# Optimization experiments

Measured on AMD Instinct MI355X. Metric: run time of the kernel, lower is better.

The kernel has to match this reference:

```python
import jax, jax.numpy as jnp
import numpy as np

N = 20000   # nodes
E = 320000  # edges
D_IN = 256
D_OUT = 256


def setup_inputs() -> dict:
    key = jax.random.key(0)
    ks = jax.random.split(key, 12)
    s = 0.05
    return {
        "h": jax.random.normal(ks[0], (N, D_OUT), jnp.float32),
        "x": jax.random.normal(ks[1], (N, D_IN), jnp.float32),
        "pos": jax.random.normal(ks[2], (N, 3), jnp.float32),
        "W_fc": jax.random.normal(ks[3], (D_OUT, D_IN + D_OUT), jnp.float32) * s,
        "b_fc": jax.random.normal(ks[4], (D_OUT,), jnp.float32) * s,
        "W_conv": jax.random.normal(ks[5], (D_OUT, D_OUT), jnp.float32) * s,
        "W_ih": jax.random.normal(ks[6], (3 * D_OUT, D_OUT), jnp.float32) * s,
        "W_hh": jax.random.normal(ks[7], (3 * D_OUT, D_OUT), jnp.float32) * s,
        "b_ih": jax.random.normal(ks[8], (3 * D_OUT,), jnp.float32) * s,
        "b_hh": jax.random.normal(ks[9], (3 * D_OUT,), jnp.float32) * s,
        "edge_index_gate": jax.random.randint(ks[10], (2, E), 0, N, jnp.int64),
        "edge_index_cand": jax.random.randint(ks[11], (2, E), 0, N, jnp.int64),
    }


def reference(h, x, pos, W_fc, b_fc, W_conv, W_ih, W_hh, b_ih, b_hh,
              edge_index_gate, edge_index_cand):
    # fc + relu on concatenated [x, h]
    xh = jnp.concatenate([x, h], axis=-1)            # [N, in+out]
    xr = jax.nn.relu(xh @ W_fc.T + b_fc)             # [N, out]

    # GatedGraphConv, num_layers=1, aggr='add'
    m = xr @ W_conv                                  # [N, out]  (x @ weight[0])
    src, dst = edge_index_gate[0], edge_index_gate[1]
    agg = jax.ops.segment_sum(m[src], dst, num_segments=xr.shape[0])  # [N, out]

    # GRUCell(agg, xr)  (torch semantics: input=agg, hidden=xr)
    gi = agg @ W_ih.T + b_ih                         # [N, 3*out]
    gh = xr @ W_hh.T + b_hh                          # [N, 3*out]
    i_r, i_z, i_n = jnp.split(gi, 3, axis=-1)
    h_r, h_z, h_n = jnp.split(gh, 3, axis=-1)
    r = jax.nn.sigmoid(i_r + h_r)
    z = jax.nn.sigmoid(i_z + h_z)
    n = jnp.tanh(i_n + r * h_n)
    h_next = (1.0 - z) * n + z * xr
    return h_next
```

## Files before the change

kernel.cpp:

```cpp
#include <hip/hip_runtime.h>
#include <hip/hip_bf16.h>

#define N_NODES 20000
#define MPAD 20032
#define CAP 64

typedef __attribute__((ext_vector_type(8))) short short8;
typedef __attribute__((ext_vector_type(4))) float f32x4;

#define MFMA16(a,b,c) __builtin_amdgcn_mfma_f32_16x16x32_bf16(a,b,c,0,0,0)

#define FSW(r) (((r) & 3) ^ (((r) >> 2) & 3))

#define WAIT_BAR(NSTR) do { \
  asm volatile("s_waitcnt vmcnt(" NSTR ") lgkmcnt(0)" ::: "memory"); \
  __builtin_amdgcn_s_barrier(); \
  __builtin_amdgcn_sched_barrier(0); \
} while (0)
#define END_BAR() do { \
  __builtin_amdgcn_sched_barrier(0); \
  __builtin_amdgcn_s_barrier(); \
} while (0)

static __device__ __forceinline__ ushort f2bf(float f) {
  union { float f; uint u; } v; v.f = f;
  uint u = v.u;
  uint r = (u + 0x7FFFu + ((u >> 16) & 1u)) >> 16;
  return (ushort)r;
}
static __device__ __forceinline__ float bf2f(ushort s) {
  union { uint u; float f; } v; v.u = ((uint)s) << 16; return v.f;
}

typedef __attribute__((address_space(1))) const unsigned int guint;
typedef __attribute__((address_space(3))) unsigned int luint;
static __device__ __forceinline__ void gl2lds16(const void* g, void* l) {
  __builtin_amdgcn_global_load_lds((guint*)g, (luint*)l, 16, 0, 0);
}

static __device__ __forceinline__ void cvt8(const float* __restrict__ s, ushort* __restrict__ d) {
  float4 v0 = *(const float4*)s;
  float4 v1 = *(const float4*)(s + 4);
  union { ushort u[8]; uint4 v; } t;
  t.u[0]=f2bf(v0.x); t.u[1]=f2bf(v0.y); t.u[2]=f2bf(v0.z); t.u[3]=f2bf(v0.w);
  t.u[4]=f2bf(v1.x); t.u[5]=f2bf(v1.y); t.u[6]=f2bf(v1.z); t.u[7]=f2bf(v1.w);
  *(uint4*)d = t.v;
}

__global__ __launch_bounds__(256) void k_prep(
    const float* __restrict__ Wfc, const float* __restrict__ Wc,
    const float* __restrict__ Wih, const float* __restrict__ Whh,
    ushort* __restrict__ WfcB, ushort* __restrict__ WcB,
    ushort* __restrict__ WihB, ushort* __restrict__ Bg3, int* __restrict__ cnt) {
  int i = blockIdx.x * 256 + threadIdx.x;
  if (i < 16384) cvt8(Wfc + i * 8, WfcB + i * 8);
  if (i < 8192)  cvt8(Wc  + i * 8, WcB  + i * 8);
  if (i < 24576) cvt8(Wih + i * 8, WihB + i * 8);
  if (i < 24576) {
    int row = i >> 5;
    int k0 = (i & 31) * 8;
    int g = row / 48, rem = row - g * 48;
    int p = rem >> 4, ci = rem & 15;
    int c = g * 16 + ci;
    cvt8(Whh + ((size_t)(p * 256 + c)) * 256 + k0, Bg3 + (size_t)row * 512 + 256 + k0);
  }
  if (i < N_NODES) cnt[i] = 0;
}

__global__ __launch_bounds__(256, 4) void k_mid(
    const float* __restrict__ x, const float* __restrict__ h,
    const ushort* __restrict__ WfcB, const float* __restrict__ bfc,
    ushort* __restrict__ AX,
    const ushort* __restrict__ WihB, const ushort* __restrict__ WcB,
    ushort* __restrict__ Bg3,
    const int* __restrict__ eg, int* __restrict__ cnt, int* __restrict__ srcs) {
  __shared__ __attribute__((aligned(16))) ushort smem[4096];
  int bid = blockIdx.x;
  int t = threadIdx.x, w = t >> 6, l = t & 63;

  if (bid >= 1304) {
    int e = (bid - 1304) * 256 + t;
    if (e < 320000) {
      int d = eg[320000 + e];
      int slot = atomicAdd(&cnt[d], 1);
      if (slot < CAP) srcs[d * CAP + slot] = eg[e];
    }
    return;
  }

  if (bid >= 1256) {
    ushort* sA = smem;
    ushort* sB = smem + 2048;
    int wf = bid - 1256;
    int row0 = (wf % 12) * 64, col0 = (wf / 12) * 64;
    int wr = (w >> 1) * 32, wc = (w & 1) * 32;
    f32x4 acc[2][2] = {};
    for (int ks = 0; ks < 8; ++ks) {
      int k0 = ks * 32;
      {
        int r = t >> 2, wl = t & 3;
        int gw = wl ^ FSW(r);
        gl2lds16(WihB + (size_t)(row0 + r) * 256 + k0 + gw * 8,
                 (char*)sA + (size_t)(w * 64) * 16);
      }
      {
        int r = t >> 2, wl = t & 3;
        int gw = wl ^ FSW(r);
        gl2lds16(WcB + (size_t)(col0 + r) * 256 + k0 + gw * 8,
                 (char*)sB + (size_t)(w * 64) * 16);
      }
      __syncthreads();
      short8 af[2], bfr[2];
      #pragma unroll
      for (int mi = 0; mi < 2; ++mi) {
        int r = wr + mi * 16 + (l & 15);
        af[mi] = *(short8*)&sA[r * 32 + (((l >> 4)) ^ FSW(r)) * 8];
      }
      #pragma unroll
      for (int ni = 0; ni < 2; ++ni) {
        int br = wc + ni * 16 + (l & 15);
        bfr[ni] = *(short8*)&sB[br * 32 + (((l >> 4)) ^ FSW(br)) * 8];
      }
      #pragma unroll
      for (int mi = 0; mi < 2; ++mi)
        #pragma unroll
        for (int ni = 0; ni < 2; ++ni)
          acc[mi][ni] = MFMA16(af[mi], bfr[ni], acc[mi][ni]);
      __syncthreads();
    }
    #pragma unroll
    for (int mi = 0; mi < 2; ++mi)
      #pragma unroll
      for (int ni = 0; ni < 2; ++ni)
        #pragma unroll
        for (int q = 0; q < 4; ++q) {
          int jj = row0 + wr + mi*16 + (l>>4)*4 + q;
          int tc = col0 + wc + ni*16 + (l&15);
          int p = jj >> 8, c = jj & 255;
          int brow = (c >> 4) * 48 + p * 16 + (c & 15);
          Bg3[(size_t)brow * 512 + tc] = f2bf(acc[mi][ni][q]);
        }
    return;
  }

  ushort* sA = smem;
  ushort* sB = smem + 2048;
  int wk = (bid & 7) * 157 + (bid >> 3);
  int panel = wk >> 2, ch = wk & 3;
  if (panel >= 313) return;
  int row0 = panel * 64, col0 = ch * 64;
  int wr = (w >> 1) * 32, wc = (w & 1) * 32;
  int r_ = t >> 2, wl_ = t & 3;
  int gw_ = wl_ ^ FSW(r_);
  int gr_ = row0 + r_; if (gr_ > N_NODES - 1) gr_ = N_NODES - 1;

  f32x4 acc[2][2] = {};
  for (int ks = 0; ks < 16; ++ks) {
    int k0 = ks * 32;
    const float* Af = (ks < 8) ? x : h;
    int ka = k0 & 255;
    {
      union { ushort u[8]; uint4 v; } tmp;
      const float* p = Af + (size_t)gr_ * 256 + ka + gw_ * 8;
      float4 v0 = *(const float4*)p;
      float4 v1 = *(const float4*)(p + 4);
      tmp.u[0]=f2bf(v0.x); tmp.u[1]=f2bf(v0.y); tmp.u[2]=f2bf(v0.z); tmp.u[3]=f2bf(v0.w);
      tmp.u[4]=f2bf(v1.x); tmp.u[5]=f2bf(v1.y); tmp.u[6]=f2bf(v1.z); tmp.u[7]=f2bf(v1.w);
      *(uint4*)&sA[r_*32 + wl_*8] = tmp.v;
    }
    gl2lds16(WfcB + (size_t)(col0 + r_) * 512 + k0 + gw_ * 8,
             (char*)sB + (size_t)(w * 64) * 16);
    __syncthreads();
    short8 af[2], bfr[2];
    #pragma unroll
    for (int mi = 0; mi < 2; ++mi) {
      int r = wr + mi * 16 + (l & 15);
      af[mi] = *(short8*)&sA[r * 32 + (((l >> 4)) ^ FSW(r)) * 8];
    }
    #pragma unroll
    for (int ni = 0; ni < 2; ++ni) {
      int br = wc + ni * 16 + (l & 15);
      bfr[ni] = *(short8*)&sB[br * 32 + (((l >> 4)) ^ FSW(br)) * 8];
    }
    #pragma unroll
    for (int mi = 0; mi < 2; ++mi)
      #pragma unroll
      for (int ni = 0; ni < 2; ++ni)
        acc[mi][ni] = MFMA16(af[mi], bfr[ni], acc[mi][ni]);
    __syncthreads();
  }
  #pragma unroll
  for (int mi = 0; mi < 2; ++mi)
    #pragma unroll
    for (int ni = 0; ni < 2; ++ni)
      #pragma unroll
      for (int q = 0; q < 4; ++q) {
        int r = row0 + wr + mi*16 + (l>>4)*4 + q;
        int c = col0 + wc + ni*16 + (l&15);
        if (r < N_NODES) {
          float v = acc[mi][ni][q] + bfc[c];
          v = v > 0.f ? v : 0.f;
          AX[(size_t)r * 512 + 256 + c] = f2bf(v);
        }
      }
}

__global__ __launch_bounds__(256) void k_aggS(
    const int* __restrict__ cnt, const int* __restrict__ srcs,
    ushort* __restrict__ AX) {
  int node = blockIdx.x * 8 + (threadIdx.x >> 5);
  if (node >= N_NODES) return;
  int lane = threadIdx.x & 31;
  const int* bkt = srcs + node * CAP;
  int n = cnt[node]; if (n > CAP) n = CAP;
  float a[8] = {};
  int i = 0;
  for (; i + 4 <= n; i += 4) {
    uint4 v0 = *(const uint4*)(AX + (size_t)bkt[i  ] * 512 + 256 + lane * 8);
    uint4 v1 = *(const uint4*)(AX + (size_t)bkt[i+1] * 512 + 256 + lane * 8);
    uint4 v2 = *(const uint4*)(AX + (size_t)bkt[i+2] * 512 + 256 + lane * 8);
    uint4 v3 = *(const uint4*)(AX + (size_t)bkt[i+3] * 512 + 256 + lane * 8);
    const ushort* p0 = (const ushort*)&v0; const ushort* p1 = (const ushort*)&v1;
    const ushort* p2 = (const ushort*)&v2; const ushort* p3 = (const ushort*)&v3;
    #pragma unroll
    for (int j = 0; j < 8; j++) a[j] += (bf2f(p0[j]) + bf2f(p1[j])) + (bf2f(p2[j]) + bf2f(p3[j]));
  }
  for (; i < n; ++i) {
    uint4 v0 = *(const uint4*)(AX + (size_t)bkt[i] * 512 + 256 + lane * 8);
    const ushort* p0 = (const ushort*)&v0;
    #pragma unroll
    for (int j = 0; j < 8; j++) a[j] += bf2f(p0[j]);
  }
  union { ushort s[8]; uint4 v; } o;
  #pragma unroll
  for (int j = 0; j < 8; j++) o.s[j] = f2bf(a[j]);
  *(uint4*)(AX + (size_t)node * 512 + lane * 8) = o.v;
}

static __device__ __forceinline__ void gru3_stage(
    const ushort* __restrict__ AX, const ushort* __restrict__ Bg3,
    ushort* sA, ushort* sB, int row0, int bro, int w, int l, int ks) {
  int k0 = ks * 64;
  #pragma unroll
  for (int j = 0; j < 2; ++j) {
    int rb = w * 16 + j * 8;
    int r = rb + (l >> 3);
    int gw = (l & 7) ^ (r & 7);
    gl2lds16(AX + (size_t)(row0 + r) * 512 + k0 + gw * 8, (char*)sA + (size_t)rb * 128);
  }
  #pragma unroll
  for (int j = 0; j < 6; ++j) {
    int rb = j * 32 + w * 8;
    int r = rb + (l >> 3);
    int gw = (l & 7) ^ (r & 7);
    gl2lds16(Bg3 + (size_t)(bro + r) * 512 + k0 + gw * 8, (char*)sB + (size_t)rb * 128);
  }
}

template<int PN>
static __device__ __forceinline__ void gru3_compute(
    const ushort* sA, const ushort* sB, int w, int l, f32x4 (&acc)[4][4]) {
  __builtin_amdgcn_s_setprio(1);
  #pragma unroll
  for (int j = 0; j < 2; ++j) {
    short8 af[4], bfr[3];
    #pragma unroll
    for (int mi = 0; mi < 4; ++mi) {
      int r = mi * 16 + (l & 15);
      af[mi] = *(const short8*)&sA[r * 64 + ((j * 4 + (l >> 4)) ^ (r & 7)) * 8];
    }
    #pragma unroll
    for (int p = 0; p < 3; ++p) {
      int br = w * 48 + p * 16 + (l & 15);
      bfr[p] = *(const short8*)&sB[br * 64 + ((j * 4 + (l >> 4)) ^ (br & 7)) * 8];
    }
    #pragma unroll
    for (int mi = 0; mi < 4; ++mi) {
      acc[mi][0]  = MFMA16(af[mi], bfr[0], acc[mi][0]);
      acc[mi][1]  = MFMA16(af[mi], bfr[1], acc[mi][1]);
      acc[mi][PN] = MFMA16(af[mi], bfr[2], acc[mi][PN]);
    }
  }
  __builtin_amdgcn_s_setprio(0);
}

__global__ __launch_bounds__(256, 2) void k_gru3(
    const ushort* __restrict__ AX, const ushort* __restrict__ Bg3,
    const float* __restrict__ bih, const float* __restrict__ bhh,
    float* __restrict__ out) {
  __shared__ __attribute__((aligned(16))) ushort smem[2 * 16384];
  ushort* sA0 = smem;
  ushort* sB0 = smem + 4096;
  ushort* sA1 = smem + 16384;
  ushort* sB1 = smem + 20480;
  int bid = blockIdx.x;
  int wk = (bid & 7) * 157 + (bid >> 3);
  int panel = wk >> 2, ch = wk & 3;
  if (panel >= 313) return;
  int row0 = panel * 64;
  int bro = ch * 192;
  int t = threadIdx.x, w = t >> 6, l = t & 63;

  gru3_stage(AX, Bg3, sA0, sB0, row0, bro, w, l, 0);
  __syncthreads();

  f32x4 acc[4][4] = {};
  #pragma unroll
  for (int ks = 0; ks < 8; ++ks) {
    ushort* cA = (ks & 1) ? sA1 : sA0;
    ushort* cB = (ks & 1) ? sB1 : sB0;
    ushort* nA = (ks & 1) ? sA0 : sA1;
    ushort* nB = (ks & 1) ? sB0 : sB1;
    if (ks < 7) gru3_stage(AX, Bg3, nA, nB, row0, bro, w, l, ks + 1);
    if (ks < 7) WAIT_BAR("8");
    else        WAIT_BAR("0");
    if (ks < 4) gru3_compute<2>(cA, cB, w, l, acc);
    else        gru3_compute<3>(cA, cB, w, l, acc);
    END_BAR();
  }

  int c = ch * 64 + w * 16 + (l & 15);
  float br_ = bih[c] + bhh[c];
  float bz_ = bih[256 + c] + bhh[256 + c];
  float bi_ = bih[512 + c];
  float bh_ = bhh[512 + c];
  #pragma unroll
  for (int mi = 0; mi < 4; ++mi)
    #pragma unroll
    for (int q = 0; q < 4; ++q) {
      int r = row0 + mi*16 + (l>>4)*4 + q;
      if (r < N_NODES) {
        float rg = 1.f / (1.f + __expf(-(acc[mi][0][q] + br_)));
        float zg = 1.f / (1.f + __expf(-(acc[mi][1][q] + bz_)));
        float ng = tanhf((acc[mi][2][q] + bi_) + rg * (acc[mi][3][q] + bh_));
        float xv = bf2f(AX[(size_t)r * 512 + 256 + c]);
        out[(size_t)r * 256 + c] = (1.f - zg) * ng + zg * xv;
      }
    }
}

extern "C" void kernel_launch(void* const* d_in, const int* in_sizes, int n_in,
                              void* d_out, int out_size, void* d_ws, size_t ws_size,
                              hipStream_t stream) {
  const float* h   = (const float*)d_in[0];
  const float* x   = (const float*)d_in[1];
  const float* Wfc = (const float*)d_in[3];
  const float* bfc = (const float*)d_in[4];
  const float* Wc  = (const float*)d_in[5];
  const float* Wih = (const float*)d_in[6];
  const float* Whh = (const float*)d_in[7];
  const float* bih = (const float*)d_in[8];
  const float* bhh = (const float*)d_in[9];
  const int*   eg  = (const int*)d_in[10];
  float* out = (float*)d_out;

  char* ws = (char*)d_ws;
  ushort* AX   = (ushort*)(ws);
  ushort* WfcB = (ushort*)(ws + 20512768);
  ushort* WcB  = (ushort*)(ws + 20774912);
  ushort* WihB = (ushort*)(ws + 20905984);
  ushort* Bg3  = (ushort*)(ws + 21299200);
  int*    cnt    = (int*)(ws + 22085632);
  int*    srcs   = (int*)(ws + 22165632);

  k_prep<<<512, 256, 0, stream>>>(Wfc, Wc, Wih, Whh, WfcB, WcB, WihB, Bg3, cnt);

  k_mid<<<2554, 256, 0, stream>>>(x, h, WfcB, bfc, AX, WihB, WcB, Bg3, eg, cnt, srcs);

  k_aggS<<<(N_NODES + 7) / 8, 256, 0, stream>>>(cnt, srcs, AX);

  k_gru3<<<1256, 256, 0, stream>>>(AX, Bg3, bih, bhh, out);
}
```

Baseline: 95.85 us.

## Fold weight conversion into k_mid and double K-tile of fc GEMM

Removes the k_prep launch. The fc, Wih and Wc weights are now converted from fp32 to bf16 inline as they are loaded into shared memory, the Whh repack runs as extra blocks inside k_mid, and the counters are cleared with a memset. The fc GEMM stages a 64-wide K slice per iteration with an 8-way XOR swizzle, which halves the number of barrier pairs. In exchange, the fc weight tile is now re-read as fp32 and re-converted by every block instead of once, and shared memory per block doubles, which may reduce occupancy.

```diff
diff --git a/kernel.cpp b/kernel.cpp
--- a/kernel.cpp
+++ b/kernel.cpp
@@ -46,45 +46,44 @@
   t.u[4]=f2bf(v1.x); t.u[5]=f2bf(v1.y); t.u[6]=f2bf(v1.z); t.u[7]=f2bf(v1.w);
   *(uint4*)d = t.v;
 }
-
-__global__ __launch_bounds__(256) void k_prep(
-    const float* __restrict__ Wfc, const float* __restrict__ Wc,
-    const float* __restrict__ Wih, const float* __restrict__ Whh,
-    ushort* __restrict__ WfcB, ushort* __restrict__ WcB,
-    ushort* __restrict__ WihB, ushort* __restrict__ Bg3, int* __restrict__ cnt) {
-  int i = blockIdx.x * 256 + threadIdx.x;
-  if (i < 16384) cvt8(Wfc + i * 8, WfcB + i * 8);
-  if (i < 8192)  cvt8(Wc  + i * 8, WcB  + i * 8);
-  if (i < 24576) cvt8(Wih + i * 8, WihB + i * 8);
-  if (i < 24576) {
+static __device__ __forceinline__ void cvt8_lds(const float* __restrict__ s, ushort* d) {
+  float4 v0 = *(const float4*)s;
+  float4 v1 = *(const float4*)(s + 4);
+  union { ushort u[8]; uint4 v; } t;
+  t.u[0]=f2bf(v0.x); t.u[1]=f2bf(v0.y); t.u[2]=f2bf(v0.z); t.u[3]=f2bf(v0.w);
+  t.u[4]=f2bf(v1.x); t.u[5]=f2bf(v1.y); t.u[6]=f2bf(v1.z); t.u[7]=f2bf(v1.w);
+  *(uint4*)d = t.v;
+}
+
+__global__ __launch_bounds__(256, 4) void k_mid(
+    const float* __restrict__ x, const float* __restrict__ h,
+    const float* __restrict__ Wfc, const float* __restrict__ bfc,
+    ushort* __restrict__ AX,
+    const float* __restrict__ Wih, const float* __restrict__ Wc,
+    const float* __restrict__ Whh, ushort* __restrict__ Bg3,
+    const int* __restrict__ eg, int* __restrict__ cnt, int* __restrict__ srcs) {
+  __shared__ __attribute__((aligned(16))) ushort smem[8192];
+  int bid = blockIdx.x;
+  int t = threadIdx.x, w = t >> 6, l = t & 63;
+
+  if (bid >= 1400) {
+    int e = (bid - 1400) * 256 + t;
+    if (e < 320000) {
+      int d = eg[320000 + e];
+      int slot = atomicAdd(&cnt[d], 1);
+      if (slot < CAP) srcs[d * CAP + slot] = eg[e];
+    }
+    return;
+  }
+
+  if (bid >= 1304) {
+    int i = (bid - 1304) * 256 + t;
     int row = i >> 5;
     int k0 = (i & 31) * 8;
     int g = row / 48, rem = row - g * 48;
     int p = rem >> 4, ci = rem & 15;
     int c = g * 16 + ci;
     cvt8(Whh + ((size_t)(p * 256 + c)) * 256 + k0, Bg3 + (size_t)row * 512 + 256 + k0);
-  }
-  if (i < N_NODES) cnt[i] = 0;
-}
-
-__global__ __launch_bounds__(256, 4) void k_mid(
-    const float* __restrict__ x, const float* __restrict__ h,
-    const ushort* __restrict__ WfcB, const float* __restrict__ bfc,
-    ushort* __restrict__ AX,
-    const ushort* __restrict__ WihB, const ushort* __restrict__ WcB,
-    ushort* __restrict__ Bg3,
-    const int* __restrict__ eg, int* __restrict__ cnt, int* __restrict__ srcs) {
-  __shared__ __attribute__((aligned(16))) ushort smem[4096];
-  int bid = blockIdx.x;
-  int t = threadIdx.x, w = t >> 6, l = t & 63;
-
-  if (bid >= 1304) {
-    int e = (bid - 1304) * 256 + t;
-    if (e < 320000) {
-      int d = eg[320000 + e];
-      int slot = atomicAdd(&cnt[d], 1);
-      if (slot < CAP) srcs[d * CAP + slot] = eg[e];
-    }
     return;
   }
 
@@ -100,14 +99,8 @@
       {
         int r = t >> 2, wl = t & 3;
         int gw = wl ^ FSW(r);
-        gl2lds16(WihB + (size_t)(row0 + r) * 256 + k0 + gw * 8,
-                 (char*)sA + (size_t)(w * 64) * 16);
-      }
-      {
-        int r = t >> 2, wl = t & 3;
-        int gw = wl ^ FSW(r);
-        gl2lds16(WcB + (size_t)(col0 + r) * 256 + k0 + gw * 8,
-                 (char*)sB + (size_t)(w * 64) * 16);
+        cvt8_lds(Wih + (size_t)(row0 + r) * 256 + k0 + gw * 8, &sA[r*32 + wl*8]);
+        cvt8_lds(Wc  + (size_t)(col0 + r) * 256 + k0 + gw * 8, &sB[r*32 + wl*8]);
       }
       __syncthreads();
       short8 af[2], bfr[2];
@@ -144,49 +137,53 @@
   }
 
   ushort* sA = smem;
-  ushort* sB = smem + 2048;
+  ushort* sB = smem + 4096;
   int wk = (bid & 7) * 157 + (bid >> 3);
   int panel = wk >> 2, ch = wk & 3;
   if (panel >= 313) return;
   int row0 = panel * 64, col0 = ch * 64;
   int wr = (w >> 1) * 32, wc = (w & 1) * 32;
-  int r_ = t >> 2, wl_ = t & 3;
-  int gw_ = wl_ ^ FSW(r_);
-  int gr_ = row0 + r_; if (gr_ > N_NODES - 1) gr_ = N_NODES - 1;
 
   f32x4 acc[2][2] = {};
-  for (int ks = 0; ks < 16; ++ks) {
-    int k0 = ks * 32;
-    const float* Af = (ks < 8) ? x : h;
+  for (int ks = 0; ks < 8; ++ks) {
+    int k0 = ks * 64;
+    const float* Af = (ks < 4) ? x : h;
     int ka = k0 & 255;
-    {
-      union { ushort u[8]; uint4 v; } tmp;
-      const float* p = Af + (size_t)gr_ * 256 + ka + gw_ * 8;
-      float4 v0 = *(const float4*)p;
-      float4 v1 = *(const float4*)(p + 4);
-      tmp.u[0]=f2bf(v0.x); tmp.u[1]=f2bf(v0.y); tmp.u[2]=f2bf(v0.z); tmp.u[3]=f2bf(v0.w);
-      tmp.u[4]=f2bf(v1.x); tmp.u[5]=f2bf(v1.y); tmp.u[6]=f2bf(v1.z); tmp.u[7]=f2bf(v1.w);
-      *(uint4*)&sA[r_*32 + wl_*8] = tmp.v;
-    }
-    gl2lds16(WfcB + (size_t)(col0 + r_) * 512 + k0 + gw_ * 8,
-             (char*)sB + (size_t)(w * 64) * 16);
+    #pragma unroll
+    for (int j = 0; j < 2; ++j) {
+      int ci = t + j * 256;
+      int r = ci >> 3, wl = ci & 7;
+      int gw = wl ^ (r & 7);
+      int gr = row0 + r; if (gr > N_NODES - 1) gr = N_NODES - 1;
+      cvt8_lds(Af + (size_t)gr * 256 + ka + gw * 8, &sA[r*64 + wl*8]);
+    }
+    #pragma unroll
+    for (int j = 0; j < 2; ++j) {
+      int ci = t + j * 256;
+      int r = ci >> 3, wl = ci & 7;
+      int gw = wl ^ (r & 7);
+      cvt8_lds(Wfc + (size_t)(col0 + r) * 512 + k0 + gw * 8, &sB[r*64 + wl*8]);
+    }
     __syncthreads();
-    short8 af[2], bfr[2];
-    #pragma unroll
-    for (int mi = 0; mi < 2; ++mi) {
-      int r = wr + mi * 16 + (l & 15);
-      af[mi] = *(short8*)&sA[r * 32 + (((l >> 4)) ^ FSW(r)) * 8];
-    }
-    #pragma unroll
-    for (int ni = 0; ni < 2; ++ni) {
-      int br = wc + ni * 16 + (l & 15);
-      bfr[ni] = *(short8*)&sB[br * 32 + (((l >> 4)) ^ FSW(br)) * 8];
-    }
-    #pragma unroll
-    for (int mi = 0; mi < 2; ++mi)
-      #pragma unroll
-      for (int ni = 0; ni < 2; ++ni)
-        acc[mi][ni] = MFMA16(af[mi], bfr[ni], acc[mi][ni]);
+    #pragma unroll
+    for (int j = 0; j < 2; ++j) {
+      short8 af[2], bfr[2];
+      #pragma unroll
+      for (int mi = 0; mi < 2; ++mi) {
+        int r = wr + mi * 16 + (l & 15);
+        af[mi] = *(short8*)&sA[r * 64 + ((j * 4 + (l >> 4)) ^ (r & 7)) * 8];
+      }
+      #pragma unroll
+      for (int ni = 0; ni < 2; ++ni) {
+        int br = wc + ni * 16 + (l & 15);
+        bfr[ni] = *(short8*)&sB[br * 64 + ((j * 4 + (l >> 4)) ^ (br & 7)) * 8];
+      }
+      #pragma unroll
+      for (int mi = 0; mi < 2; ++mi)
+        #pragma unroll
+        for (int ni = 0; ni < 2; ++ni)
+          acc[mi][ni] = MFMA16(af[mi], bfr[ni], acc[mi][ni]);
+    }
     __syncthreads();
   }
   #pragma unroll
@@ -356,16 +353,13 @@
 
   char* ws = (char*)d_ws;
   ushort* AX   = (ushort*)(ws);
-  ushort* WfcB = (ushort*)(ws + 20512768);
-  ushort* WcB  = (ushort*)(ws + 20774912);
-  ushort* WihB = (ushort*)(ws + 20905984);
-  ushort* Bg3  = (ushort*)(ws + 21299200);
-  int*    cnt    = (int*)(ws + 22085632);
-  int*    srcs   = (int*)(ws + 22165632);
-
-  k_prep<<<512, 256, 0, stream>>>(Wfc, Wc, Wih, Whh, WfcB, WcB, WihB, Bg3, cnt);
-
-  k_mid<<<2554, 256, 0, stream>>>(x, h, WfcB, bfc, AX, WihB, WcB, Bg3, eg, cnt, srcs);
+  ushort* Bg3  = (ushort*)(ws + 20512768);
+  int*    cnt    = (int*)(ws + 21299200);
+  int*    srcs   = (int*)(ws + 21379200);
+
+  hipMemsetAsync(cnt, 0, (size_t)N_NODES * 4, stream);
+
+  k_mid<<<2650, 256, 0, stream>>>(x, h, Wfc, bfc, AX, Wih, Wc, Whh, Bg3, eg, cnt, srcs);
 
   k_aggS<<<(N_NODES + 7) / 8, 256, 0, stream>>>(cnt, srcs, AX);
 
```

After: 88.78 us (median of 3 runs). -7.4%, faster.
